# Performance work log

Hardware: AMD Instinct MI355X
Metric: run time of the kernel (lower is better)

Reference implementation:

```python
import jax, jax.numpy as jnp
import numpy as np

WINDOW_SIZE = 11
SIGMA = 1.5
C3 = 1e-4
EPS = 1e-12


def _gaussian_window(channels):
    # 1D Gaussian, normalized, then outer product -> 2D separable window
    coords = jnp.arange(WINDOW_SIZE, dtype=jnp.float32) - WINDOW_SIZE // 2
    g = jnp.exp(-coords ** 2 / (2.0 * SIGMA ** 2))
    g = g / g.sum()
    w2 = g[:, None] * g[None, :]                      # [K, K]
    return jnp.broadcast_to(w2, (channels, 1, WINDOW_SIZE, WINDOW_SIZE))


def _dwconv(x, w, channels):
    # depthwise (groups=C) 2D conv with SAME-style symmetric zero padding
    pad = WINDOW_SIZE // 2
    return jax.lax.conv_general_dilated(
        x, w,
        window_strides=(1, 1),
        padding=[(pad, pad), (pad, pad)],
        dimension_numbers=('NCHW', 'OIHW', 'NCHW'),
        feature_group_count=channels,
    )


def reference(x, y):
    x = x.astype(jnp.float32)
    y = y.astype(jnp.float32)
    N, C = x.shape[0], x.shape[1]
    w = _gaussian_window(C)
    mu_x = _dwconv(x, w, C)
    mu_y = _dwconv(y, w, C)
    sigma_xy = _dwconv(x * y, w, C) - mu_x * mu_y
    sigma_x = jnp.clip(_dwconv(x * x, w, C) - mu_x * mu_x, EPS, None)
    sigma_y = jnp.clip(_dwconv(y * y, w, C) - mu_y * mu_y, EPS, None)
    structure = (sigma_xy + C3) / (jnp.sqrt(sigma_x) * jnp.sqrt(sigma_y) + C3)
    structure_mean = structure.reshape(N, C, -1).mean(axis=2)  # [N, C]
    loss = (1.0 - structure_mean).mean()
    return loss


def setup_inputs() -> dict:
    key = jax.random.key(0)
    kx, ky = jax.random.split(key)
    x = jax.random.uniform(kx, (8, 3, 512, 512), dtype=jnp.float32)
    y = jax.random.uniform(ky, (8, 3, 512, 512), dtype=jnp.float32)
    return {"x": x, "y": y}
```

## Files before the change

kernel.cpp:

```cpp
#include <hip/hip_runtime.h>

#define IMG_H 512
#define IMG_W 512
#define NPLANES 24
#define ROWS_PER_BLK 16
#define STRIPW 512
#define NITER 26
#define NBLOCKS (32 * 24)
#define TOTAL_PIX 6291456.0f

typedef float f32x2 __attribute__((ext_vector_type(2)));

__device__ __constant__ float GW[11] = {
    0.00102838f, 0.00759876f, 0.03600050f, 0.10935817f, 0.21300535f,
    0.26601172f, 0.21300535f, 0.10935817f, 0.03600050f, 0.00759876f,
    0.00102838f};

extern "C" __global__ __launch_bounds__(512) void ssim_structure_kernel(
    const float* __restrict__ x, const float* __restrict__ y,
    float* __restrict__ accum, unsigned int* __restrict__ counter,
    float* __restrict__ out) {
  const int tid = threadIdx.x;
  const int chunk = blockIdx.x;
  const int plane = blockIdx.y;

  const size_t pbase = (size_t)plane * IMG_H * IMG_W;
  const float* __restrict__ xp = x + pbase;
  const float* __restrict__ yp = y + pbase;
  const int r0 = chunk * ROWS_PER_BLK;

  __shared__ f32x2 lrow[2][STRIPW + 16];

  f32x2 bm[11];
  f32x2 bq[11];
  float bxy[11];

  float acc = 0.0f;

  const int gc = tid - 5;
  const int gcc = min(max(gc, 0), IMG_W - 1);
  const float cmask = (gc >= 0 && gc < IMG_W) ? 1.0f : 0.0f;
  const int gc2 = gc + STRIPW;
  const int gc2c = min(gc2, IMG_W - 1);
  const float hmask = (gc2 < IMG_W) ? 1.0f : 0.0f;

  f32x2 pre_m, pre_e;
  pre_m = (f32x2){0.f, 0.f};
  pre_e = (f32x2){0.f, 0.f};

  auto loadrow = [&](int i, f32x2& m, f32x2& e) {
    const int hr = r0 - 5 + i;
    if ((i < NITER) & (hr >= 0) & (hr < IMG_H)) {
      const int rowoff = hr * IMG_W;
      f32x2 v;
      v.x = xp[rowoff + gcc];
      v.y = yp[rowoff + gcc];
      m = v * cmask;
      if (tid < 10) {
        f32x2 h;
        h.x = xp[rowoff + gc2c];
        h.y = yp[rowoff + gc2c];
        e = h * hmask;
      }
    } else {
      m = (f32x2){0.f, 0.f};
      e = (f32x2){0.f, 0.f};
    }
  };

  loadrow(0, pre_m, pre_e);

  for (int ob = 0; ob < 3; ++ob) {
#pragma unroll
    for (int ii = 0; ii < 11; ++ii) {
      const int i = ob * 11 + ii;
      if (i < NITER) {
        const int sel = i & 1;

        lrow[sel][tid] = pre_m;
        if (tid < 10) lrow[sel][STRIPW + tid] = pre_e;

        loadrow(i + 1, pre_m, pre_e);

        __syncthreads();

        {
          f32x2 tm = {0.f, 0.f};
          f32x2 tq = {0.f, 0.f};
          float txy = 0.f;
#pragma unroll
          for (int d = 0; d < 11; ++d) {
            const f32x2 v = lrow[sel][tid + d];
            const float w = GW[d];
            const f32x2 wv = v * w;
            tm += wv;
            tq = __builtin_elementwise_fma(wv, v, tq);
            txy = fmaf(wv.x, v.y, txy);
          }
          bm[ii] = tm;
          bq[ii] = tq;
          bxy[ii] = txy;
        }

        if (i >= 10) {
          f32x2 vm = {0.f, 0.f};
          f32x2 vq = {0.f, 0.f};
          float vxy = 0.f;
#pragma unroll
          for (int k = 0; k < 11; ++k) {
            const int s = (ii + 1 + k) % 11;
            const float w = GW[k];
            const f32x2 w2 = {w, w};
            vm = __builtin_elementwise_fma(bm[s], w2, vm);
            vq = __builtin_elementwise_fma(bq[s], w2, vq);
            vxy = fmaf(w, bxy[s], vxy);
          }
          const float sxy = fmaf(-vm.x, vm.y, vxy);
          f32x2 sp = __builtin_elementwise_fma(-vm, vm, vq);
          sp = __builtin_elementwise_max(sp, (f32x2){1e-12f, 1e-12f});
          const float denom = sqrtf(sp.x) * sqrtf(sp.y) + 1e-4f;
          acc += (sxy + 1e-4f) / denom;
        }
      }
    }
  }

#pragma unroll
  for (int off = 32; off > 0; off >>= 1) acc += __shfl_down(acc, off, 64);
  __shared__ float wsum[8];
  if ((tid & 63) == 0) wsum[tid >> 6] = acc;
  __syncthreads();
  if (tid == 0) {
    float bsum = 0.f;
#pragma unroll
    for (int w = 0; w < 8; ++w) bsum += wsum[w];
    atomicAdd(accum, bsum);
    __threadfence();
    const unsigned int ret = atomicAdd(counter, 1u);
    if (ret == (unsigned int)(NBLOCKS - 1)) {
      __threadfence();
      const float total = atomicAdd(accum, 0.0f);
      out[0] = 1.0f - total * (1.0f / TOTAL_PIX);
    }
  }
}

extern "C" void kernel_launch(void* const* d_in, const int* in_sizes, int n_in,
                              void* d_out, int out_size, void* d_ws,
                              size_t ws_size, hipStream_t stream) {
  const float* x = (const float*)d_in[0];
  const float* y = (const float*)d_in[1];
  float* out = (float*)d_out;
  float* accum = (float*)d_ws;
  unsigned int* counter = (unsigned int*)((char*)d_ws + sizeof(float));

  hipMemsetAsync(d_ws, 0, 2 * sizeof(float), stream);

  dim3 grid(IMG_H / ROWS_PER_BLK, NPLANES);
  ssim_structure_kernel<<<grid, 512, 0, stream>>>(x, y, accum, counter, out);
}
```

Baseline: 140.3 us.

## Give each wavefront its own column strip with private halo, dropping block barriers

Each 64-lane wavefront now owns a 64-column strip and loads its own 10-column halo into a per-wave double-buffered LDS row. Because every LDS row is produced and consumed by the same wavefront, the per-row __syncthreads is removed. Blocks shrink to 256 threads, and the grid gains a column-group dimension so the whole image is still covered. In exchange, halo columns are loaded redundantly at every wave boundary, and correctness relies on lockstep execution within a wavefront with no explicit wave barrier.

After: 147.2 us. 4.9% more time.

```diff
diff --git a/kernel.cpp b/kernel.cpp
--- a/kernel.cpp
+++ b/kernel.cpp
@@ -4,9 +4,9 @@
 #define IMG_W 512
 #define NPLANES 24
 #define ROWS_PER_BLK 16
-#define STRIPW 512
 #define NITER 26
-#define NBLOCKS (32 * 24)
+#define NWAVES 4
+#define NBLOCKS (32 * 2 * 24)
 #define TOTAL_PIX 6291456.0f
 
 typedef float f32x2 __attribute__((ext_vector_type(2)));
@@ -16,20 +16,24 @@
     0.26601172f, 0.21300535f, 0.10935817f, 0.03600050f, 0.00759876f,
     0.00102838f};
 
-extern "C" __global__ __launch_bounds__(512) void ssim_structure_kernel(
+extern "C" __global__ __launch_bounds__(256) void ssim_structure_kernel(
     const float* __restrict__ x, const float* __restrict__ y,
     float* __restrict__ accum, unsigned int* __restrict__ counter,
     float* __restrict__ out) {
   const int tid = threadIdx.x;
-  const int chunk = blockIdx.x;
-  const int plane = blockIdx.y;
+  const int lane = tid & 63;
+  const int w = tid >> 6;
+  const int band = blockIdx.x;
+  const int sgrp = blockIdx.y;
+  const int plane = blockIdx.z;
 
   const size_t pbase = (size_t)plane * IMG_H * IMG_W;
   const float* __restrict__ xp = x + pbase;
   const float* __restrict__ yp = y + pbase;
-  const int r0 = chunk * ROWS_PER_BLK;
+  const int cbase = (sgrp * NWAVES + w) * 64;
+  const int r0 = band * ROWS_PER_BLK;
 
-  __shared__ f32x2 lrow[2][STRIPW + 16];
+  __shared__ f32x2 lrow[NWAVES][2][80];
 
   f32x2 bm[11];
   f32x2 bq[11];
@@ -37,16 +41,14 @@
 
   float acc = 0.0f;
 
-  const int gc = tid - 5;
+  const int gc = cbase - 5 + lane;
   const int gcc = min(max(gc, 0), IMG_W - 1);
   const float cmask = (gc >= 0 && gc < IMG_W) ? 1.0f : 0.0f;
-  const int gc2 = gc + STRIPW;
+  const int gc2 = cbase + 59 + lane;
   const int gc2c = min(gc2, IMG_W - 1);
   const float hmask = (gc2 < IMG_W) ? 1.0f : 0.0f;
 
-  f32x2 pre_m, pre_e;
-  pre_m = (f32x2){0.f, 0.f};
-  pre_e = (f32x2){0.f, 0.f};
+  f32x2 pre_m = {0.f, 0.f}, pre_e = {0.f, 0.f};
 
   auto loadrow = [&](int i, f32x2& m, f32x2& e) {
     const int hr = r0 - 5 + i;
@@ -56,7 +58,7 @@
       v.x = xp[rowoff + gcc];
       v.y = yp[rowoff + gcc];
       m = v * cmask;
-      if (tid < 10) {
+      if (lane < 10) {
         f32x2 h;
         h.x = xp[rowoff + gc2c];
         h.y = yp[rowoff + gc2c];
@@ -77,12 +79,10 @@
       if (i < NITER) {
         const int sel = i & 1;
 
-        lrow[sel][tid] = pre_m;
-        if (tid < 10) lrow[sel][STRIPW + tid] = pre_e;
+        lrow[w][sel][lane] = pre_m;
+        if (lane < 10) lrow[w][sel][64 + lane] = pre_e;
 
         loadrow(i + 1, pre_m, pre_e);
-
-        __syncthreads();
 
         {
           f32x2 tm = {0.f, 0.f};
@@ -90,9 +90,9 @@
           float txy = 0.f;
 #pragma unroll
           for (int d = 0; d < 11; ++d) {
-            const f32x2 v = lrow[sel][tid + d];
-            const float w = GW[d];
-            const f32x2 wv = v * w;
+            const f32x2 v = lrow[w][sel][lane + d];
+            const float wgt = GW[d];
+            const f32x2 wv = v * wgt;
             tm += wv;
             tq = __builtin_elementwise_fma(wv, v, tq);
             txy = fmaf(wv.x, v.y, txy);
@@ -109,11 +109,11 @@
 #pragma unroll
           for (int k = 0; k < 11; ++k) {
             const int s = (ii + 1 + k) % 11;
-            const float w = GW[k];
-            const f32x2 w2 = {w, w};
+            const float wgt = GW[k];
+            const f32x2 w2 = {wgt, wgt};
             vm = __builtin_elementwise_fma(bm[s], w2, vm);
             vq = __builtin_elementwise_fma(bq[s], w2, vq);
-            vxy = fmaf(w, bxy[s], vxy);
+            vxy = fmaf(wgt, bxy[s], vxy);
           }
           const float sxy = fmaf(-vm.x, vm.y, vxy);
           f32x2 sp = __builtin_elementwise_fma(-vm, vm, vq);
@@ -127,13 +127,13 @@
 
 #pragma unroll
   for (int off = 32; off > 0; off >>= 1) acc += __shfl_down(acc, off, 64);
-  __shared__ float wsum[8];
-  if ((tid & 63) == 0) wsum[tid >> 6] = acc;
+  __shared__ float wsum[NWAVES];
+  if (lane == 0) wsum[w] = acc;
   __syncthreads();
   if (tid == 0) {
     float bsum = 0.f;
 #pragma unroll
-    for (int w = 0; w < 8; ++w) bsum += wsum[w];
+    for (int v = 0; v < NWAVES; ++v) bsum += wsum[v];
     atomicAdd(accum, bsum);
     __threadfence();
     const unsigned int ret = atomicAdd(counter, 1u);
@@ -156,6 +156,6 @@
 
   hipMemsetAsync(d_ws, 0, 2 * sizeof(float), stream);
 
-  dim3 grid(IMG_H / ROWS_PER_BLK, NPLANES);
-  ssim_structure_kernel<<<grid, 512, 0, stream>>>(x, y, accum, counter, out);
+  dim3 grid(IMG_H / ROWS_PER_BLK, 2, NPLANES);
+  ssim_structure_kernel<<<grid, 256, 0, stream>>>(x, y, accum, counter, out);
 }
```

## Compute two output columns per thread with float4 LDS rows and deeper prefetch

Applied to the files above, without the earlier changes.

Each thread now handles two adjacent columns, so the block shrinks to 256 threads and loads float2 vectors from global memory. Rows are staged in LDS as interleaved float4 (x,y pairs) with zero halos, which lets the horizontal pass share loaded taps between the two outputs. Row prefetch goes three rows deep instead of one, and the Gaussian weights become compile-time constants. The per-pixel divide is replaced by a fast reciprocal and a single sqrt of the product. In exchange the register arrays double in size, which may lower occupancy, and rcpf is slightly less accurate than a true divide.

New measurement: 213.5 us. +52.1%, slower.

```diff
diff --git a/kernel.cpp b/kernel.cpp
--- a/kernel.cpp
+++ b/kernel.cpp
@@ -4,136 +4,147 @@
 #define IMG_W 512
 #define NPLANES 24
 #define ROWS_PER_BLK 16
-#define STRIPW 512
 #define NITER 26
 #define NBLOCKS (32 * 24)
 #define TOTAL_PIX 6291456.0f
 
 typedef float f32x2 __attribute__((ext_vector_type(2)));
+typedef float f32x4 __attribute__((ext_vector_type(4)));
 
-__device__ __constant__ float GW[11] = {
+constexpr float GWc[11] = {
     0.00102838f, 0.00759876f, 0.03600050f, 0.10935817f, 0.21300535f,
     0.26601172f, 0.21300535f, 0.10935817f, 0.03600050f, 0.00759876f,
     0.00102838f};
 
-extern "C" __global__ __launch_bounds__(512) void ssim_structure_kernel(
+extern "C" __global__ __launch_bounds__(256) void ssim_structure_kernel(
     const float* __restrict__ x, const float* __restrict__ y,
     float* __restrict__ accum, unsigned int* __restrict__ counter,
     float* __restrict__ out) {
   const int tid = threadIdx.x;
-  const int chunk = blockIdx.x;
+  const int band = blockIdx.x;
   const int plane = blockIdx.y;
 
   const size_t pbase = (size_t)plane * IMG_H * IMG_W;
   const float* __restrict__ xp = x + pbase;
   const float* __restrict__ yp = y + pbase;
-  const int r0 = chunk * ROWS_PER_BLK;
+  const int r0 = band * ROWS_PER_BLK;
+  const int c0 = tid * 2;
 
-  __shared__ f32x2 lrow[2][STRIPW + 16];
+  __shared__ f32x4 lrow[2][264];
 
-  f32x2 bm[11];
-  f32x2 bq[11];
-  float bxy[11];
+  if (tid < 16) {
+    const int b = tid >> 3, k = tid & 7;
+    lrow[b][(k < 4) ? k : (256 + k)] = (f32x4){0.f, 0.f, 0.f, 0.f};
+  }
+
+  f32x2 bm0[11], bq0[11], bm1[11], bq1[11];
+  float bxy0[11], bxy1[11];
+
+  f32x2 ax[3], ay[3];
 
   float acc = 0.0f;
 
-  const int gc = tid - 5;
-  const int gcc = min(max(gc, 0), IMG_W - 1);
-  const float cmask = (gc >= 0 && gc < IMG_W) ? 1.0f : 0.0f;
-  const int gc2 = gc + STRIPW;
-  const int gc2c = min(gc2, IMG_W - 1);
-  const float hmask = (gc2 < IMG_W) ? 1.0f : 0.0f;
-
-  f32x2 pre_m, pre_e;
-  pre_m = (f32x2){0.f, 0.f};
-  pre_e = (f32x2){0.f, 0.f};
-
-  auto loadrow = [&](int i, f32x2& m, f32x2& e) {
+  auto loadrow = [&](int i, f32x2& vx, f32x2& vy) {
     const int hr = r0 - 5 + i;
-    if ((i < NITER) & (hr >= 0) & (hr < IMG_H)) {
-      const int rowoff = hr * IMG_W;
-      f32x2 v;
-      v.x = xp[rowoff + gcc];
-      v.y = yp[rowoff + gcc];
-      m = v * cmask;
-      if (tid < 10) {
-        f32x2 h;
-        h.x = xp[rowoff + gc2c];
-        h.y = yp[rowoff + gc2c];
-        e = h * hmask;
-      }
+    if ((i < NITER) && (hr >= 0) && (hr < IMG_H)) {
+      const int off = hr * IMG_W + c0;
+      vx = *reinterpret_cast<const f32x2*>(xp + off);
+      vy = *reinterpret_cast<const f32x2*>(yp + off);
     } else {
-      m = (f32x2){0.f, 0.f};
-      e = (f32x2){0.f, 0.f};
+      vx = (f32x2){0.f, 0.f};
+      vy = (f32x2){0.f, 0.f};
     }
   };
 
-  loadrow(0, pre_m, pre_e);
+  loadrow(0, ax[0], ay[0]);
+  loadrow(1, ax[1], ay[1]);
+  loadrow(2, ax[2], ay[2]);
 
-  for (int ob = 0; ob < 3; ++ob) {
 #pragma unroll
-    for (int ii = 0; ii < 11; ++ii) {
-      const int i = ob * 11 + ii;
-      if (i < NITER) {
-        const int sel = i & 1;
+  for (int i = 0; i < NITER; ++i) {
+    const int s = i % 3;
+    const int sel = i & 1;
+    const int ii = i % 11;
 
-        lrow[sel][tid] = pre_m;
-        if (tid < 10) lrow[sel][STRIPW + tid] = pre_e;
+    f32x4 st;
+    st.x = ax[s].x; st.y = ay[s].x;
+    st.z = ax[s].y; st.w = ay[s].y;
+    lrow[sel][4 + tid] = st;
 
-        loadrow(i + 1, pre_m, pre_e);
+    loadrow(i + 3, ax[s], ay[s]);
 
-        __syncthreads();
+    __syncthreads();
 
-        {
-          f32x2 tm = {0.f, 0.f};
-          f32x2 tq = {0.f, 0.f};
-          float txy = 0.f;
+    f32x2 tm0 = {0.f, 0.f}, tq0 = {0.f, 0.f};
+    f32x2 tm1 = {0.f, 0.f}, tq1 = {0.f, 0.f};
+    float txy0 = 0.f, txy1 = 0.f;
+
+    auto tap = [&](const f32x2 v, int j) {
+      if (j >= 1 && j <= 11) {
+        const float w = GWc[j - 1];
+        const f32x2 wv = v * w;
+        tm0 += wv;
+        tq0 = __builtin_elementwise_fma(wv, v, tq0);
+        txy0 = fmaf(wv.x, v.y, txy0);
+      }
+      if (j >= 2 && j <= 12) {
+        const float w = GWc[j - 2];
+        const f32x2 wv = v * w;
+        tm1 += wv;
+        tq1 = __builtin_elementwise_fma(wv, v, tq1);
+        txy1 = fmaf(wv.x, v.y, txy1);
+      }
+    };
+
 #pragma unroll
-          for (int d = 0; d < 11; ++d) {
-            const f32x2 v = lrow[sel][tid + d];
-            const float w = GW[d];
-            const f32x2 wv = v * w;
-            tm += wv;
-            tq = __builtin_elementwise_fma(wv, v, tq);
-            txy = fmaf(wv.x, v.y, txy);
-          }
-          bm[ii] = tm;
-          bq[ii] = tq;
-          bxy[ii] = txy;
-        }
+    for (int k = 0; k < 7; ++k) {
+      const f32x4 q = lrow[sel][1 + tid + k];
+      tap((f32x2){q.x, q.y}, 2 * k);
+      tap((f32x2){q.z, q.w}, 2 * k + 1);
+    }
+    bm0[ii] = tm0; bq0[ii] = tq0; bxy0[ii] = txy0;
+    bm1[ii] = tm1; bq1[ii] = tq1; bxy1[ii] = txy1;
 
-        if (i >= 10) {
-          f32x2 vm = {0.f, 0.f};
-          f32x2 vq = {0.f, 0.f};
-          float vxy = 0.f;
+    if (i >= 10) {
+      f32x2 vm0 = {0.f, 0.f}, vq0 = {0.f, 0.f};
+      f32x2 vm1 = {0.f, 0.f}, vq1 = {0.f, 0.f};
+      float vxy0 = 0.f, vxy1 = 0.f;
 #pragma unroll
-          for (int k = 0; k < 11; ++k) {
-            const int s = (ii + 1 + k) % 11;
-            const float w = GW[k];
-            const f32x2 w2 = {w, w};
-            vm = __builtin_elementwise_fma(bm[s], w2, vm);
-            vq = __builtin_elementwise_fma(bq[s], w2, vq);
-            vxy = fmaf(w, bxy[s], vxy);
-          }
-          const float sxy = fmaf(-vm.x, vm.y, vxy);
-          f32x2 sp = __builtin_elementwise_fma(-vm, vm, vq);
-          sp = __builtin_elementwise_max(sp, (f32x2){1e-12f, 1e-12f});
-          const float denom = sqrtf(sp.x) * sqrtf(sp.y) + 1e-4f;
-          acc += (sxy + 1e-4f) / denom;
-        }
+      for (int k = 0; k < 11; ++k) {
+        const int s2 = (ii + 1 + k) % 11;
+        const float w = GWc[k];
+        const f32x2 w2 = {w, w};
+        vm0 = __builtin_elementwise_fma(bm0[s2], w2, vm0);
+        vq0 = __builtin_elementwise_fma(bq0[s2], w2, vq0);
+        vxy0 = fmaf(w, bxy0[s2], vxy0);
+        vm1 = __builtin_elementwise_fma(bm1[s2], w2, vm1);
+        vq1 = __builtin_elementwise_fma(bq1[s2], w2, vq1);
+        vxy1 = fmaf(w, bxy1[s2], vxy1);
+      }
+      {
+        const float sxy = fmaf(-vm0.x, vm0.y, vxy0);
+        f32x2 sp = __builtin_elementwise_fma(-vm0, vm0, vq0);
+        sp = __builtin_elementwise_max(sp, (f32x2){1e-12f, 1e-12f});
+        const float den = sqrtf(sp.x * sp.y) + 1e-4f;
+        acc = fmaf(sxy + 1e-4f, __builtin_amdgcn_rcpf(den), acc);
+      }
+      {
+        const float sxy = fmaf(-vm1.x, vm1.y, vxy1);
+        f32x2 sp = __builtin_elementwise_fma(-vm1, vm1, vq1);
+        sp = __builtin_elementwise_max(sp, (f32x2){1e-12f, 1e-12f});
+        const float den = sqrtf(sp.x * sp.y) + 1e-4f;
+        acc = fmaf(sxy + 1e-4f, __builtin_amdgcn_rcpf(den), acc);
       }
     }
   }
 
 #pragma unroll
   for (int off = 32; off > 0; off >>= 1) acc += __shfl_down(acc, off, 64);
-  __shared__ float wsum[8];
+  __shared__ float wsum[4];
   if ((tid & 63) == 0) wsum[tid >> 6] = acc;
   __syncthreads();
   if (tid == 0) {
-    float bsum = 0.f;
-#pragma unroll
-    for (int w = 0; w < 8; ++w) bsum += wsum[w];
+    float bsum = wsum[0] + wsum[1] + wsum[2] + wsum[3];
     atomicAdd(accum, bsum);
     __threadfence();
     const unsigned int ret = atomicAdd(counter, 1u);
@@ -157,5 +168,5 @@
   hipMemsetAsync(d_ws, 0, 2 * sizeof(float), stream);
 
   dim3 grid(IMG_H / ROWS_PER_BLK, NPLANES);
-  ssim_structure_kernel<<<grid, 512, 0, stream>>>(x, y, accum, counter, out);
+  ssim_structure_kernel<<<grid, 256, 0, stream>>>(x, y, accum, counter, out);
 }
```
